# Kernel tuning notes

Measured on AMD Instinct MI355X. Metric: run time of the kernel, lower is better.

## Reference

```python
import jax, jax.numpy as jnp
import numpy as np

N, B, D, K, H = 30000, 16, 32, 8, 8
DIST = 5.0
EPS = 1e-6


def setup_inputs() -> dict:
    key = jax.random.key(0)
    ks = jax.random.split(key, 16)
    sc = 1.0 / np.sqrt(D)
    inp = {
        'pos': jax.random.uniform(ks[0], (N, 3), jnp.float32) * 20.0,
        'node_features': jax.random.normal(ks[1], (N, D), jnp.float32),
        'batch': jnp.sort(jax.random.randint(ks[2], (N,), 0, B, dtype=jnp.int32)),
        'bessel_weights': jnp.linspace(jnp.pi, K * jnp.pi, K).astype(jnp.float32),
        'init_dummy': jax.random.normal(ks[3], (D,), jnp.float32),
        'Wq_dummy': jax.random.normal(ks[4], (D, D), jnp.float32) * sc,
        'Wq_graph': jax.random.normal(ks[5], (D, D), jnp.float32) * sc,
        'Wdot': jax.random.normal(ks[6], (D, D), jnp.float32) * sc,
        'W1_kd': jax.random.normal(ks[7], (K, H), jnp.float32) / np.sqrt(K),
        'W2_kd': jax.random.normal(ks[8], (H, D * D), jnp.float32) / np.sqrt(H),
        'W1_vd': jax.random.normal(ks[9], (K, H), jnp.float32) / np.sqrt(K),
        'W2_vd': jax.random.normal(ks[10], (H, D * D), jnp.float32) / np.sqrt(H),
        'W1_kg': jax.random.normal(ks[11], (K, H), jnp.float32) / np.sqrt(K),
        'W2_kg': jax.random.normal(ks[12], (H, D * D), jnp.float32) / np.sqrt(H),
        'W1_vg': jax.random.normal(ks[13], (K, H), jnp.float32) / np.sqrt(K),
        'W2_vg': jax.random.normal(ks[14], (H, D * D), jnp.float32) / np.sqrt(H),
    }
    return inp


def reference(pos, node_features, batch, bessel_weights, init_dummy,
              Wq_dummy, Wq_graph, Wdot,
              W1_kd, W2_kd, W1_vd, W2_vd, W1_kg, W2_kg, W1_vg, W2_vg):
    scale = 1.0 / np.sqrt(D)

    # --- dummy edge features: per-batch z extents + bessel basis ---
    z = pos[:, 2]                                            # [N]
    z_min = jax.ops.segment_min(z, batch, num_segments=B)    # [B]
    z_max = jax.ops.segment_max(z, batch, num_segments=B)    # [B]
    bot_len = z - z_min[batch] + DIST                        # [N]
    top_len = z_max[batch] + DIST - z                        # [N]

    def bessel(x):  # [N] -> [N,K]
        return jnp.sin(bessel_weights * x[:, None]) / (x[:, None] + EPS)

    edge = jnp.stack([bessel(bot_len), bessel(top_len)], axis=1)  # [N,2,K]

    # --- init dummy node features [B, 2, D] ---
    dummy = jnp.broadcast_to(init_dummy, (B, 2, D))

    def gen_w(W1, W2):  # conditional weight generator (silu MLP)
        return (jax.nn.silu(edge @ W1) @ W2).reshape(N, 2, D, D)

    # --- dummy nodes attend over graph nodes (segment softmax) ---
    wk = gen_w(W1_kd, W2_kd)                                 # [N,2,D,D]
    wv = gen_w(W1_vd, W2_vd)
    q = (dummy @ Wq_dummy)[batch]                            # [N,2,D]
    k = jnp.einsum('nd,nsde->nse', node_features, wk)        # [N,2,D]
    v = jnp.einsum('nd,nsde->nse', node_features, wv)
    s = jnp.einsum('nsq,qk,nsk->ns', q, Wdot, k) * scale     # [N,2]
    m = jax.ops.segment_max(s, batch, num_segments=B)
    e = jnp.exp(s - m[batch])
    zsum = jax.ops.segment_sum(e, batch, num_segments=B)
    attn = e / zsum[batch]                                   # [N,2]
    dummy_new = dummy + jax.ops.segment_sum(attn[..., None] * v, batch, num_segments=B)

    # --- graph nodes attend over (2) dummy nodes ---
    wkg = gen_w(W1_kg, W2_kg)
    wvg = gen_w(W1_vg, W2_vg)
    d_per = dummy_new[batch]                                 # [N,2,D]
    kg = jnp.einsum('nsd,nsde->nse', d_per, wkg)
    vg = jnp.einsum('nsd,nsde->nse', d_per, wvg)
    qg = node_features @ Wq_graph                            # [N,D]
    sg = jnp.einsum('nq,qk,nsk->ns', qg, Wdot, kg) * scale   # [N,2]
    ag = jax.nn.softmax(sg, axis=1)
    x_new = node_features + jnp.einsum('ns,nsd->nd', ag, vg)  # [N,D]
    return x_new
```

## Files before the change

kernel.cpp:

```cpp
#include <hip/hip_runtime.h>
#include <math.h>

#define NN 30000
#define DIST_C 5.0f
#define EPS_C 1e-6f
#define SCALE_C 0.17677669529663687f

#define WS_ZMIN 0
#define WS_ZMAX 16
#define WS_ZSUM 32
#define WS_T    64
#define WS_PK   8256
#define WS_WC   8512

__device__ __forceinline__ float silu(float x) { return x / (1.0f + expf(-x)); }

__device__ __forceinline__ void bessel_edges(float bw0, float x0, float x1, float edge[2][8]) {
    float xs[2]; xs[0] = x0; xs[1] = x1;
#pragma unroll
    for (int s = 0; s < 2; ++s) {
        float x = xs[s];
        float inv = 1.0f / (x + EPS_C);
        float th = bw0 * x;
        float c2 = 2.0f * cosf(th);
        float skm1 = 0.0f;
        float sk = sinf(th);
#pragma unroll
        for (int k = 0; k < 8; ++k) {
            edge[s][k] = sk * inv;
            float nx = c2 * sk - skm1;
            skm1 = sk; sk = nx;
        }
    }
}

__global__ __launch_bounds__(256) void k_pre(const float* __restrict__ pos,
                                             const int* __restrict__ batch,
                                             const float* __restrict__ init_dummy,
                                             const float* __restrict__ Wq_dummy,
                                             const float* __restrict__ Wdot,
                                             const float* __restrict__ W2_kd,
                                             const float* __restrict__ Wq_graph,
                                             float* __restrict__ ws) {
    int t = threadIdx.x, blk = blockIdx.x;
    if (blk < 16) {
        __shared__ int bnd2[2];
        __shared__ float r[8];
        if (t < 2) {
            int target = blk + t;
            int lo = 0, hi = NN;
            while (lo < hi) { int mid = (lo + hi) >> 1; if (batch[mid] < target) lo = mid + 1; else hi = mid; }
            bnd2[t] = lo;
        }
        __syncthreads();
        int s0 = bnd2[0], s1 = bnd2[1];
        float zmn = 3.4e38f, zmx = -3.4e38f;
        for (int i = s0 + t; i < s1; i += 256) {
            float v = pos[3 * i + 2];
            zmn = fminf(zmn, v); zmx = fmaxf(zmx, v);
        }
#pragma unroll
        for (int off = 1; off < 64; off <<= 1) {
            zmn = fminf(zmn, __shfl_xor(zmn, off, 64));
            zmx = fmaxf(zmx, __shfl_xor(zmx, off, 64));
        }
        if ((t & 63) == 0) { r[(t >> 6) * 2] = zmn; r[(t >> 6) * 2 + 1] = zmx; }
        __syncthreads();
        if (t == 0) {
            ws[WS_ZMIN + blk] = fminf(fminf(r[0], r[2]), fminf(r[4], r[6]));
            ws[WS_ZMAX + blk] = fmaxf(fmaxf(r[1], r[3]), fmaxf(r[5], r[7]));
        }
    } else if (blk == 16) {
        __shared__ float qv[32], qW[32];
        if (t < 32) {
            float acc = 0.f;
            for (int d = 0; d < 32; ++d) acc += init_dummy[d] * Wq_dummy[d * 32 + t];
            qv[t] = acc;
        }
        __syncthreads();
        if (t < 32) {
            float acc = 0.f;
            for (int e = 0; e < 32; ++e) acc += qv[e] * Wdot[e * 32 + t];
            qW[t] = acc;
        }
        __syncthreads();
        int h = t >> 5, d = t & 31;
        float acc = 0.f;
        for (int e = 0; e < 32; ++e) acc += W2_kd[h * 1024 + d * 32 + e] * qW[e];
        ws[WS_PK + t] = acc;
    } else if (blk == 17) {
        for (int i = t; i < 1024; i += 256) {
            int d = i >> 5, e = i & 31;
            float acc = 0.f;
            for (int m = 0; m < 32; ++m) acc += Wq_graph[d * 32 + m] * Wdot[m * 32 + e];
            ws[WS_WC + i] = acc;
        }
    } else {
        int idx = blk - 18;
        ws[WS_T + idx * 512 + t] = 0.f;
        ws[WS_T + idx * 512 + 256 + t] = 0.f;
        if (idx == 0 && t < 32) ws[WS_ZSUM + t] = 0.f;
    }
}

__global__ __launch_bounds__(256) void k_phase1(const float* __restrict__ pos,
                                                const int* __restrict__ batch,
                                                const float* __restrict__ nf,
                                                const float* __restrict__ bw,
                                                const float* __restrict__ W1_kd,
                                                const float* __restrict__ W1_vd,
                                                float* __restrict__ ws) {
    __shared__ __align__(16) float Fl[32 * 36];
    __shared__ float Lw[32 * 17];
    __shared__ int   Lb[32];
    __shared__ __align__(16) float Pk[256];
    __shared__ float W1kd[64], W1vd[64], zsl[32];
    int t = threadIdx.x;
    if (t < 64) { W1kd[t] = W1_kd[t]; W1vd[t] = W1_vd[t]; }
    Pk[t] = ws[WS_PK + t];
    if (t < 32) zsl[t] = 0.f;

    int li = t >> 3, g = t & 7;
    int n0 = blockIdx.x * 32;
    int n = n0 + li;
    bool valid = n < NN;
    float4 fv4 = make_float4(0.f, 0.f, 0.f, 0.f);
    int b = 0;
    if (valid) {
        b = batch[n];
        fv4 = ((const float4*)nf)[n * 8 + g];
        ((float4*)(Fl + li * 36))[g] = fv4;
        if (g == 0) Lb[li] = b;
    } else {
        if (g == 0) Lb[li] = -1;
    }
    __syncthreads();

    if (valid) {
        float z = pos[3 * n + 2];
        float zminb = ws[WS_ZMIN + b];
        float zmaxb = ws[WS_ZMAX + b];
        float edge[2][8];
        bessel_edges(bw[0], z - zminb + DIST_C, zmaxb + DIST_C - z, edge);

        float up[8];
        const float4* Pk4 = (const float4*)Pk;
#pragma unroll
        for (int h = 0; h < 8; ++h) {
            float4 p = Pk4[h * 8 + g];
            up[h] = fv4.x * p.x + fv4.y * p.y + fv4.z * p.z + fv4.w * p.w;
        }
        float kd0, kd1;
        {
            float p0 = 0.f, p1 = 0.f;
#pragma unroll
            for (int k = 0; k < 8; ++k) {
                float w = W1kd[k * 8 + g];
                p0 += edge[0][k] * w;
                p1 += edge[1][k] * w;
            }
            kd0 = silu(p0); kd1 = silu(p1);
        }
        int lanebase = (t & 63) & 56;
        float sp0 = 0.f, sp1 = 0.f;
#pragma unroll
        for (int h = 0; h < 8; ++h) {
            sp0 += __shfl(kd0, lanebase + h, 64) * up[h];
            sp1 += __shfl(kd1, lanebase + h, 64) * up[h];
        }
#pragma unroll
        for (int m = 1; m < 8; m <<= 1) {
            sp0 += __shfl_xor(sp0, m, 64);
            sp1 += __shfl_xor(sp1, m, 64);
        }
        float ev0 = expf(sp0 * SCALE_C);
        float ev1 = expf(sp1 * SCALE_C);
        if (g == 0) {
            atomicAdd(&zsl[b * 2 + 0], ev0);
            atomicAdd(&zsl[b * 2 + 1], ev1);
        }
        float q0 = 0.f, q1 = 0.f;
#pragma unroll
        for (int k = 0; k < 8; ++k) {
            float w = W1vd[k * 8 + g];
            q0 += edge[0][k] * w;
            q1 += edge[1][k] * w;
        }
        Lw[li * 17 + g]     = ev0 * silu(q0);
        Lw[li * 17 + 8 + g] = ev1 * silu(q1);
    }
    __syncthreads();
    if (t < 32 && zsl[t] != 0.f) atomicAdd(&ws[WS_ZSUM + t], zsl[t]);

    int count = NN - n0; if (count > 32) count = 32;
    int bf = Lb[0], bl = Lb[count - 1];
    int sh = t & 15, dp = t >> 4;
    for (int b2 = bf; b2 <= bl; ++b2) {
        float a0 = 0.f, a1 = 0.f;
        for (int i = 0; i < count; ++i) {
            if (Lb[i] != b2) continue;
            float w = Lw[i * 17 + sh];
            float2 x = *(const float2*)(Fl + i * 36 + 2 * dp);
            a0 += w * x.x;
            a1 += w * x.y;
        }
        float* Tb = ws + WS_T + b2 * 512 + sh * 32 + 2 * dp;
        atomicAdd(&Tb[0], a0);
        atomicAdd(&Tb[1], a1);
    }
}

__global__ __launch_bounds__(256) void k_fin(const float* __restrict__ pos,
                                             const int* __restrict__ batch,
                                             const float* __restrict__ nf,
                                             const float* __restrict__ bw,
                                             const float* __restrict__ W1_kg,
                                             const float* __restrict__ W1_vg,
                                             const float* __restrict__ init_dummy,
                                             const float* __restrict__ W2_vd,
                                             const float* __restrict__ W2_kg,
                                             const float* __restrict__ W2_vg,
                                             const float* __restrict__ ws,
                                             float* __restrict__ out) {
    __shared__ __align__(16) float Wc[1024];
    __shared__ __align__(16) float Fl[32 * 36];
    __shared__ int   Lb[32];
    __shared__ float W1kg[64], W1vg[64];
    __shared__ float Tl[2][512];
    __shared__ float part[2][512];
    __shared__ float dn[2][64];
    __shared__ __align__(16) float AK[2][512], AV[2][512];

    int t = threadIdx.x;
    int li = t >> 3, g = t & 7;
    int lanebase = (t & 63) & 56;
    for (int i = t; i < 1024; i += 256) Wc[i] = ws[WS_WC + i];
    if (t < 64) { W1kg[t] = W1_kg[t]; W1vg[t] = W1_vg[t]; }

    int n0 = blockIdx.x * 32;
    int n = n0 + li;
    int count = NN - n0; if (count > 32) count = 32;
    bool valid = li < count;
    float4 fv4 = make_float4(0.f, 0.f, 0.f, 0.f);
    float z = 0.f;
    int b = 0;
    if (valid) {
        b = batch[n];
        fv4 = ((const float4*)nf)[n * 8 + g];
        ((float4*)(Fl + li * 36))[g] = fv4;
        z = pos[3 * n + 2];
        if (g == 0) Lb[li] = b;
    }
    __syncthreads();
    int bf = Lb[0], bl = Lb[count - 1];

    Tl[0][t]       = ws[WS_T + bf * 512 + t];
    Tl[0][256 + t] = ws[WS_T + bf * 512 + 256 + t];
    Tl[1][t]       = ws[WS_T + bl * 512 + t];
    Tl[1][256 + t] = ws[WS_T + bl * 512 + 256 + t];
    __syncthreads();
    {
        int h = t >> 5, e = t & 31;
        float a00 = 0.f, a01 = 0.f, a10 = 0.f, a11 = 0.f;
        for (int d = 0; d < 32; ++d) {
            float w2 = W2_vd[h * 1024 + d * 32 + e];
            a00 += Tl[0][h * 32 + d] * w2;
            a01 += Tl[0][256 + h * 32 + d] * w2;
            a10 += Tl[1][h * 32 + d] * w2;
            a11 += Tl[1][256 + h * 32 + d] * w2;
        }
        part[0][t] = a00; part[0][256 + t] = a01;
        part[1][t] = a10; part[1][256 + t] = a11;
    }
    __syncthreads();
    if (t < 64) {
        int s = t >> 5, dd = t & 31;
        float acc0 = 0.f, acc1 = 0.f;
        for (int h = 0; h < 8; ++h) {
            acc0 += part[0][s * 256 + h * 32 + dd];
            acc1 += part[1][s * 256 + h * 32 + dd];
        }
        float id = init_dummy[dd];
        dn[0][t] = id + acc0 / ws[WS_ZSUM + bf * 2 + s];
        dn[1][t] = id + acc1 / ws[WS_ZSUM + bl * 2 + s];
    }
    __syncthreads();
    {
        int h = t >> 5, e = t & 31;
        float k00 = 0.f, k01 = 0.f, k10 = 0.f, k11 = 0.f;
        float v00 = 0.f, v01 = 0.f, v10 = 0.f, v11 = 0.f;
        for (int d = 0; d < 32; ++d) {
            float w2k = W2_kg[h * 1024 + d * 32 + e];
            float w2v = W2_vg[h * 1024 + d * 32 + e];
            k00 += dn[0][d] * w2k;      v00 += dn[0][d] * w2v;
            k01 += dn[0][32 + d] * w2k; v01 += dn[0][32 + d] * w2v;
            k10 += dn[1][d] * w2k;      v10 += dn[1][d] * w2v;
            k11 += dn[1][32 + d] * w2k; v11 += dn[1][32 + d] * w2v;
        }
        AK[0][t] = k00; AK[0][256 + t] = k01;
        AK[1][t] = k10; AK[1][256 + t] = k11;
        AV[0][t] = v00; AV[0][256 + t] = v01;
        AV[1][t] = v10; AV[1][256 + t] = v11;
    }
    __syncthreads();

    if (!valid) return;
    int slot = (b == bf) ? 0 : 1;
    const float4* Ak4 = (const float4*)AK[slot];
    const float4* Av4 = (const float4*)AV[slot];
    const float4* Wc4 = (const float4*)Wc;

    float zminb = ws[WS_ZMIN + b];
    float zmaxb = ws[WS_ZMAX + b];
    float edge[2][8];
    bessel_edges(bw[0], z - zminb + DIST_C, zmaxb + DIST_C - z, edge);

    float sk0, sk1, sv0, sv1;
    {
        float pk0 = 0.f, pk1 = 0.f, pv0 = 0.f, pv1 = 0.f;
#pragma unroll
        for (int k = 0; k < 8; ++k) {
            float wk = W1kg[k * 8 + g];
            float wv = W1vg[k * 8 + g];
            pk0 += edge[0][k] * wk; pk1 += edge[1][k] * wk;
            pv0 += edge[0][k] * wv; pv1 += edge[1][k] * wv;
        }
        sk0 = silu(pk0); sk1 = silu(pk1);
        sv0 = silu(pv0); sv1 = silu(pv1);
    }
    float4 q4 = make_float4(0.f, 0.f, 0.f, 0.f);
    const float* myF = Fl + li * 36;
#pragma unroll
    for (int d = 0; d < 32; ++d) {
        float fd = myF[d];
        float4 w = Wc4[d * 8 + g];
        q4.x += fd * w.x; q4.y += fd * w.y; q4.z += fd * w.z; q4.w += fd * w.w;
    }
    float p0 = 0.f, p1 = 0.f;
#pragma unroll
    for (int h = 0; h < 8; ++h) {
        float4 a0 = Ak4[h * 8 + g];
        float4 a1 = Ak4[64 + h * 8 + g];
        float d0 = q4.x * a0.x + q4.y * a0.y + q4.z * a0.z + q4.w * a0.w;
        float d1 = q4.x * a1.x + q4.y * a1.y + q4.z * a1.z + q4.w * a1.w;
        p0 += __shfl(sk0, lanebase + h, 64) * d0;
        p1 += __shfl(sk1, lanebase + h, 64) * d1;
    }
#pragma unroll
    for (int m = 1; m < 8; m <<= 1) {
        p0 += __shfl_xor(p0, m, 64);
        p1 += __shfl_xor(p1, m, 64);
    }
    float sg0 = p0 * SCALE_C, sg1 = p1 * SCALE_C;
    float mx = fmaxf(sg0, sg1);
    float e0 = expf(sg0 - mx), e1 = expf(sg1 - mx);
    float inv = 1.0f / (e0 + e1);
    float ag0 = e0 * inv, ag1 = e1 * inv;

    float4 x4 = fv4;
#pragma unroll
    for (int h = 0; h < 8; ++h) {
        float w0 = ag0 * __shfl(sv0, lanebase + h, 64);
        float w1 = ag1 * __shfl(sv1, lanebase + h, 64);
        float4 a0 = Av4[h * 8 + g];
        float4 a1 = Av4[64 + h * 8 + g];
        x4.x += w0 * a0.x + w1 * a1.x;
        x4.y += w0 * a0.y + w1 * a1.y;
        x4.z += w0 * a0.z + w1 * a1.z;
        x4.w += w0 * a0.w + w1 * a1.w;
    }
    ((float4*)out)[n * 8 + g] = x4;
}

extern "C" void kernel_launch(void* const* d_in, const int* in_sizes, int n_in,
                              void* d_out, int out_size, void* d_ws, size_t ws_size,
                              hipStream_t stream) {
    const float* pos        = (const float*)d_in[0];
    const float* nf         = (const float*)d_in[1];
    const int*   batch      = (const int*)d_in[2];
    const float* bw         = (const float*)d_in[3];
    const float* init_dummy = (const float*)d_in[4];
    const float* Wq_dummy   = (const float*)d_in[5];
    const float* Wq_graph   = (const float*)d_in[6];
    const float* Wdot       = (const float*)d_in[7];
    const float* W1_kd      = (const float*)d_in[8];
    const float* W2_kd      = (const float*)d_in[9];
    const float* W1_vd      = (const float*)d_in[10];
    const float* W2_vd      = (const float*)d_in[11];
    const float* W1_kg      = (const float*)d_in[12];
    const float* W2_kg      = (const float*)d_in[13];
    const float* W1_vg      = (const float*)d_in[14];
    const float* W2_vg      = (const float*)d_in[15];
    float* ws  = (float*)d_ws;
    float* out = (float*)d_out;

    int nblk = (NN + 31) / 32;
    hipLaunchKernelGGL(k_pre, dim3(34), dim3(256), 0, stream,
                       pos, batch, init_dummy, Wq_dummy, Wdot, W2_kd, Wq_graph, ws);
    hipLaunchKernelGGL(k_phase1, dim3(nblk), dim3(256), 0, stream,
                       pos, batch, nf, bw, W1_kd, W1_vd, ws);
    hipLaunchKernelGGL(k_fin, dim3(nblk), dim3(256), 0, stream,
                       pos, batch, nf, bw, W1_kg, W1_vg, init_dummy,
                       W2_vd, W2_kg, W2_vg, ws, out);
}
```

Baseline: 124.0 us.

## Halve node tile per block and skip duplicate dummy-segment recompute

Both the phase1 and final kernels now handle 16 nodes per block with 128 threads instead of 32 nodes with 256 threads. This doubles the grid size, and bounds checks are dropped because N divides evenly by 16. The final kernel computes the per-block dummy-node chain (T·W2_vd, then dn, then K/V through W2_kg/W2_vg) only for the segments actually present, usually one instead of always two. It reuses two scratch buffers in place of four shared arrays, which cuts shared memory. The phase1 scatter now uses float4 loads and four atomics per thread. The trade-off is that more blocks each redo the per-segment matvec work, so total redundant weight reads may rise even though each block does less.

```diff
diff --git a/kernel.cpp b/kernel.cpp
--- a/kernel.cpp
+++ b/kernel.cpp
@@ -12,6 +12,8 @@
 #define WS_T    64
 #define WS_PK   8256
 #define WS_WC   8512
+
+#define NPT 16
 
 __device__ __forceinline__ float silu(float x) { return x / (1.0f + expf(-x)); }
 
@@ -103,40 +105,34 @@
     }
 }
 
-__global__ __launch_bounds__(256) void k_phase1(const float* __restrict__ pos,
+__global__ __launch_bounds__(128) void k_phase1(const float* __restrict__ pos,
                                                 const int* __restrict__ batch,
                                                 const float* __restrict__ nf,
                                                 const float* __restrict__ bw,
                                                 const float* __restrict__ W1_kd,
                                                 const float* __restrict__ W1_vd,
                                                 float* __restrict__ ws) {
-    __shared__ __align__(16) float Fl[32 * 36];
-    __shared__ float Lw[32 * 17];
-    __shared__ int   Lb[32];
+    __shared__ __align__(16) float Fl[NPT * 36];
+    __shared__ float Lw[NPT * 17];
+    __shared__ int   Lb[NPT];
     __shared__ __align__(16) float Pk[256];
     __shared__ float W1kd[64], W1vd[64], zsl[32];
     int t = threadIdx.x;
     if (t < 64) { W1kd[t] = W1_kd[t]; W1vd[t] = W1_vd[t]; }
     Pk[t] = ws[WS_PK + t];
+    Pk[t + 128] = ws[WS_PK + t + 128];
     if (t < 32) zsl[t] = 0.f;
 
     int li = t >> 3, g = t & 7;
-    int n0 = blockIdx.x * 32;
+    int n0 = blockIdx.x * NPT;
     int n = n0 + li;
-    bool valid = n < NN;
-    float4 fv4 = make_float4(0.f, 0.f, 0.f, 0.f);
-    int b = 0;
-    if (valid) {
-        b = batch[n];
-        fv4 = ((const float4*)nf)[n * 8 + g];
-        ((float4*)(Fl + li * 36))[g] = fv4;
-        if (g == 0) Lb[li] = b;
-    } else {
-        if (g == 0) Lb[li] = -1;
-    }
-    __syncthreads();
-
-    if (valid) {
+    int b = batch[n];
+    float4 fv4 = ((const float4*)nf)[n * 8 + g];
+    ((float4*)(Fl + li * 36))[g] = fv4;
+    if (g == 0) Lb[li] = b;
+    __syncthreads();
+
+    {
         float z = pos[3 * n + 2];
         float zminb = ws[WS_ZMIN + b];
         float zmaxb = ws[WS_ZMAX + b];
@@ -192,25 +188,24 @@
     __syncthreads();
     if (t < 32 && zsl[t] != 0.f) atomicAdd(&ws[WS_ZSUM + t], zsl[t]);
 
-    int count = NN - n0; if (count > 32) count = 32;
-    int bf = Lb[0], bl = Lb[count - 1];
-    int sh = t & 15, dp = t >> 4;
+    int bf = Lb[0], bl = Lb[NPT - 1];
+    int sh = t & 15, dq = t >> 4;
+    const float4* Fl4 = (const float4*)Fl;
     for (int b2 = bf; b2 <= bl; ++b2) {
-        float a0 = 0.f, a1 = 0.f;
-        for (int i = 0; i < count; ++i) {
+        float4 a = make_float4(0.f, 0.f, 0.f, 0.f);
+        for (int i = 0; i < NPT; ++i) {
             if (Lb[i] != b2) continue;
             float w = Lw[i * 17 + sh];
-            float2 x = *(const float2*)(Fl + i * 36 + 2 * dp);
-            a0 += w * x.x;
-            a1 += w * x.y;
-        }
-        float* Tb = ws + WS_T + b2 * 512 + sh * 32 + 2 * dp;
-        atomicAdd(&Tb[0], a0);
-        atomicAdd(&Tb[1], a1);
-    }
-}
-
-__global__ __launch_bounds__(256) void k_fin(const float* __restrict__ pos,
+            float4 x = Fl4[i * 9 + dq];
+            a.x += w * x.x; a.y += w * x.y; a.z += w * x.z; a.w += w * x.w;
+        }
+        float* Tb = ws + WS_T + b2 * 512 + sh * 32 + dq * 4;
+        atomicAdd(&Tb[0], a.x); atomicAdd(&Tb[1], a.y);
+        atomicAdd(&Tb[2], a.z); atomicAdd(&Tb[3], a.w);
+    }
+}
+
+__global__ __launch_bounds__(128) void k_fin(const float* __restrict__ pos,
                                              const int* __restrict__ batch,
                                              const float* __restrict__ nf,
                                              const float* __restrict__ bw,
@@ -223,91 +218,87 @@
                                              const float* __restrict__ ws,
                                              float* __restrict__ out) {
     __shared__ __align__(16) float Wc[1024];
-    __shared__ __align__(16) float Fl[32 * 36];
-    __shared__ int   Lb[32];
+    __shared__ __align__(16) float Fl[NPT * 36];
+    __shared__ int   Lb[NPT];
     __shared__ float W1kg[64], W1vg[64];
-    __shared__ float Tl[2][512];
-    __shared__ float part[2][512];
+    __shared__ __align__(16) float scr0[2][512];
+    __shared__ __align__(16) float scr1[2][512];
     __shared__ float dn[2][64];
-    __shared__ __align__(16) float AK[2][512], AV[2][512];
 
     int t = threadIdx.x;
     int li = t >> 3, g = t & 7;
     int lanebase = (t & 63) & 56;
-    for (int i = t; i < 1024; i += 256) Wc[i] = ws[WS_WC + i];
+    {
+        const float4* Wg4 = (const float4*)(ws + WS_WC);
+        float4* Wc4w = (float4*)Wc;
+        Wc4w[t] = Wg4[t];
+        Wc4w[t + 128] = Wg4[t + 128];
+    }
     if (t < 64) { W1kg[t] = W1_kg[t]; W1vg[t] = W1_vg[t]; }
 
-    int n0 = blockIdx.x * 32;
+    int n0 = blockIdx.x * NPT;
     int n = n0 + li;
-    int count = NN - n0; if (count > 32) count = 32;
-    bool valid = li < count;
-    float4 fv4 = make_float4(0.f, 0.f, 0.f, 0.f);
-    float z = 0.f;
-    int b = 0;
-    if (valid) {
-        b = batch[n];
-        fv4 = ((const float4*)nf)[n * 8 + g];
-        ((float4*)(Fl + li * 36))[g] = fv4;
-        z = pos[3 * n + 2];
-        if (g == 0) Lb[li] = b;
-    }
-    __syncthreads();
-    int bf = Lb[0], bl = Lb[count - 1];
-
-    Tl[0][t]       = ws[WS_T + bf * 512 + t];
-    Tl[0][256 + t] = ws[WS_T + bf * 512 + 256 + t];
-    Tl[1][t]       = ws[WS_T + bl * 512 + t];
-    Tl[1][256 + t] = ws[WS_T + bl * 512 + 256 + t];
-    __syncthreads();
-    {
-        int h = t >> 5, e = t & 31;
-        float a00 = 0.f, a01 = 0.f, a10 = 0.f, a11 = 0.f;
-        for (int d = 0; d < 32; ++d) {
-            float w2 = W2_vd[h * 1024 + d * 32 + e];
-            a00 += Tl[0][h * 32 + d] * w2;
-            a01 += Tl[0][256 + h * 32 + d] * w2;
-            a10 += Tl[1][h * 32 + d] * w2;
-            a11 += Tl[1][256 + h * 32 + d] * w2;
-        }
-        part[0][t] = a00; part[0][256 + t] = a01;
-        part[1][t] = a10; part[1][256 + t] = a11;
+    int b = batch[n];
+    float4 fv4 = ((const float4*)nf)[n * 8 + g];
+    ((float4*)(Fl + li * 36))[g] = fv4;
+    float z = pos[3 * n + 2];
+    if (g == 0) Lb[li] = b;
+    __syncthreads();
+    int bf = Lb[0], bl = Lb[NPT - 1];
+    int nseg = (bl != bf) ? 2 : 1;
+
+    for (int sl = 0; sl < nseg; ++sl) {
+        const float* Tg = ws + WS_T + (sl ? bl : bf) * 512;
+        scr0[sl][t]       = Tg[t];
+        scr0[sl][t + 128] = Tg[t + 128];
+        scr0[sl][t + 256] = Tg[t + 256];
+        scr0[sl][t + 384] = Tg[t + 384];
+    }
+    __syncthreads();
+    for (int sl = 0; sl < nseg; ++sl) {
+        for (int o = t; o < 256; o += 128) {
+            int h = o >> 5, e = o & 31;
+            float a0 = 0.f, a1 = 0.f;
+            for (int d = 0; d < 32; ++d) {
+                float w2 = W2_vd[h * 1024 + d * 32 + e];
+                a0 += scr0[sl][h * 32 + d] * w2;
+                a1 += scr0[sl][256 + h * 32 + d] * w2;
+            }
+            scr1[sl][o] = a0; scr1[sl][256 + o] = a1;
+        }
     }
     __syncthreads();
     if (t < 64) {
         int s = t >> 5, dd = t & 31;
-        float acc0 = 0.f, acc1 = 0.f;
-        for (int h = 0; h < 8; ++h) {
-            acc0 += part[0][s * 256 + h * 32 + dd];
-            acc1 += part[1][s * 256 + h * 32 + dd];
-        }
         float id = init_dummy[dd];
-        dn[0][t] = id + acc0 / ws[WS_ZSUM + bf * 2 + s];
-        dn[1][t] = id + acc1 / ws[WS_ZSUM + bl * 2 + s];
-    }
-    __syncthreads();
-    {
-        int h = t >> 5, e = t & 31;
-        float k00 = 0.f, k01 = 0.f, k10 = 0.f, k11 = 0.f;
-        float v00 = 0.f, v01 = 0.f, v10 = 0.f, v11 = 0.f;
-        for (int d = 0; d < 32; ++d) {
-            float w2k = W2_kg[h * 1024 + d * 32 + e];
-            float w2v = W2_vg[h * 1024 + d * 32 + e];
-            k00 += dn[0][d] * w2k;      v00 += dn[0][d] * w2v;
-            k01 += dn[0][32 + d] * w2k; v01 += dn[0][32 + d] * w2v;
-            k10 += dn[1][d] * w2k;      v10 += dn[1][d] * w2v;
-            k11 += dn[1][32 + d] * w2k; v11 += dn[1][32 + d] * w2v;
-        }
-        AK[0][t] = k00; AK[0][256 + t] = k01;
-        AK[1][t] = k10; AK[1][256 + t] = k11;
-        AV[0][t] = v00; AV[0][256 + t] = v01;
-        AV[1][t] = v10; AV[1][256 + t] = v11;
-    }
-    __syncthreads();
-
-    if (!valid) return;
+        for (int sl = 0; sl < nseg; ++sl) {
+            int bb = sl ? bl : bf;
+            float acc = 0.f;
+            for (int h = 0; h < 8; ++h) acc += scr1[sl][s * 256 + h * 32 + dd];
+            dn[sl][t] = id + acc / ws[WS_ZSUM + bb * 2 + s];
+        }
+    }
+    __syncthreads();
+    for (int sl = 0; sl < nseg; ++sl) {
+        for (int o = t; o < 256; o += 128) {
+            int h = o >> 5, e = o & 31;
+            float k0 = 0.f, k1 = 0.f, v0 = 0.f, v1 = 0.f;
+            for (int d = 0; d < 32; ++d) {
+                float w2k = W2_kg[h * 1024 + d * 32 + e];
+                float w2v = W2_vg[h * 1024 + d * 32 + e];
+                float d0 = dn[sl][d], d1 = dn[sl][32 + d];
+                k0 += d0 * w2k; k1 += d1 * w2k;
+                v0 += d0 * w2v; v1 += d1 * w2v;
+            }
+            scr0[sl][o] = k0; scr0[sl][256 + o] = k1;
+            scr1[sl][o] = v0; scr1[sl][256 + o] = v1;
+        }
+    }
+    __syncthreads();
+
     int slot = (b == bf) ? 0 : 1;
-    const float4* Ak4 = (const float4*)AK[slot];
-    const float4* Av4 = (const float4*)AV[slot];
+    const float4* Ak4 = (const float4*)scr0[slot];
+    const float4* Av4 = (const float4*)scr1[slot];
     const float4* Wc4 = (const float4*)Wc;
 
     float zminb = ws[WS_ZMIN + b];
@@ -394,12 +385,12 @@
     float* ws  = (float*)d_ws;
     float* out = (float*)d_out;
 
-    int nblk = (NN + 31) / 32;
+    int nblk = NN / NPT;
     hipLaunchKernelGGL(k_pre, dim3(34), dim3(256), 0, stream,
                        pos, batch, init_dummy, Wq_dummy, Wdot, W2_kd, Wq_graph, ws);
-    hipLaunchKernelGGL(k_phase1, dim3(nblk), dim3(256), 0, stream,
+    hipLaunchKernelGGL(k_phase1, dim3(nblk), dim3(128), 0, stream,
                        pos, batch, nf, bw, W1_kd, W1_vd, ws);
-    hipLaunchKernelGGL(k_fin, dim3(nblk), dim3(256), 0, stream,
+    hipLaunchKernelGGL(k_fin, dim3(nblk), dim3(128), 0, stream,
                        pos, batch, nf, bw, W1_kg, W1_vg, init_dummy,
                        W2_vd, W2_kg, W2_vg, ws, out);
 }
```

Result: slower. 154.6 us (+24.7%).

## Hoist per-batch dummy-node K/V computation into a separate small kernel

Applied to the files above, without the earlier changes.

The per-batch dummy update and the graph-side K/V projections were recomputed redundantly in every k_fin block (about 938 blocks, each doing matvecs against W2_vd, W2_kg and W2_vg). They are now computed once per (batch, side) pair by a new 32-block k_batch kernel, which stores them in the workspace. k_fin only loads the one or two precomputed 512-float slices it needs, and the Wc load becomes a float4 copy. This adds one extra kernel launch and a global round trip in exchange for removing the redundant weight reads and FLOPs.

```diff
diff --git a/kernel.cpp b/kernel.cpp
--- a/kernel.cpp
+++ b/kernel.cpp
@@ -12,6 +12,10 @@
 #define WS_T    64
 #define WS_PK   8256
 #define WS_WC   8512
+#define WS_AKG  9536
+#define WS_AVG  17728
+
+#define NPT 32
 
 __device__ __forceinline__ float silu(float x) { return x / (1.0f + expf(-x)); }
 
@@ -110,9 +114,9 @@
                                                 const float* __restrict__ W1_kd,
                                                 const float* __restrict__ W1_vd,
                                                 float* __restrict__ ws) {
-    __shared__ __align__(16) float Fl[32 * 36];
-    __shared__ float Lw[32 * 17];
-    __shared__ int   Lb[32];
+    __shared__ __align__(16) float Fl[NPT * 36];
+    __shared__ float Lw[NPT * 17];
+    __shared__ int   Lb[NPT];
     __shared__ __align__(16) float Pk[256];
     __shared__ float W1kd[64], W1vd[64], zsl[32];
     int t = threadIdx.x;
@@ -121,7 +125,7 @@
     if (t < 32) zsl[t] = 0.f;
 
     int li = t >> 3, g = t & 7;
-    int n0 = blockIdx.x * 32;
+    int n0 = blockIdx.x * NPT;
     int n = n0 + li;
     bool valid = n < NN;
     float4 fv4 = make_float4(0.f, 0.f, 0.f, 0.f);
@@ -192,7 +196,7 @@
     __syncthreads();
     if (t < 32 && zsl[t] != 0.f) atomicAdd(&ws[WS_ZSUM + t], zsl[t]);
 
-    int count = NN - n0; if (count > 32) count = 32;
+    int count = NN - n0; if (count > NPT) count = NPT;
     int bf = Lb[0], bl = Lb[count - 1];
     int sh = t & 15, dp = t >> 4;
     for (int b2 = bf; b2 <= bl; ++b2) {
@@ -210,36 +214,75 @@
     }
 }
 
+__global__ __launch_bounds__(256) void k_batch(const float* __restrict__ init_dummy,
+                                               const float* __restrict__ W2_vd,
+                                               const float* __restrict__ W2_kg,
+                                               const float* __restrict__ W2_vg,
+                                               float* __restrict__ ws) {
+    int bs = blockIdx.x;
+    int b = bs >> 1, s = bs & 1;
+    int t = threadIdx.x;
+    __shared__ float Tl[256];
+    __shared__ float part[256];
+    __shared__ float dn[32];
+    Tl[t] = ws[WS_T + b * 512 + s * 256 + t];
+    __syncthreads();
+    {
+        int h = t >> 5, e = t & 31;
+        float acc = 0.f;
+#pragma unroll
+        for (int d = 0; d < 32; ++d) acc += Tl[h * 32 + d] * W2_vd[h * 1024 + d * 32 + e];
+        part[t] = acc;
+    }
+    __syncthreads();
+    if (t < 32) {
+        float acc = 0.f;
+#pragma unroll
+        for (int h = 0; h < 8; ++h) acc += part[h * 32 + t];
+        float zs = ws[WS_ZSUM + b * 2 + s];
+        dn[t] = init_dummy[t] + acc / zs;
+    }
+    __syncthreads();
+    {
+        int h = t >> 5, e = t & 31;
+        float ak = 0.f, av = 0.f;
+#pragma unroll
+        for (int d = 0; d < 32; ++d) {
+            float dv = dn[d];
+            ak += dv * W2_kg[h * 1024 + d * 32 + e];
+            av += dv * W2_vg[h * 1024 + d * 32 + e];
+        }
+        ws[WS_AKG + b * 512 + s * 256 + t] = ak;
+        ws[WS_AVG + b * 512 + s * 256 + t] = av;
+    }
+}
+
 __global__ __launch_bounds__(256) void k_fin(const float* __restrict__ pos,
                                              const int* __restrict__ batch,
                                              const float* __restrict__ nf,
                                              const float* __restrict__ bw,
                                              const float* __restrict__ W1_kg,
                                              const float* __restrict__ W1_vg,
-                                             const float* __restrict__ init_dummy,
-                                             const float* __restrict__ W2_vd,
-                                             const float* __restrict__ W2_kg,
-                                             const float* __restrict__ W2_vg,
                                              const float* __restrict__ ws,
                                              float* __restrict__ out) {
     __shared__ __align__(16) float Wc[1024];
-    __shared__ __align__(16) float Fl[32 * 36];
-    __shared__ int   Lb[32];
+    __shared__ __align__(16) float Fl[NPT * 36];
+    __shared__ int   Lb[NPT];
     __shared__ float W1kg[64], W1vg[64];
-    __shared__ float Tl[2][512];
-    __shared__ float part[2][512];
-    __shared__ float dn[2][64];
     __shared__ __align__(16) float AK[2][512], AV[2][512];
 
     int t = threadIdx.x;
     int li = t >> 3, g = t & 7;
     int lanebase = (t & 63) & 56;
-    for (int i = t; i < 1024; i += 256) Wc[i] = ws[WS_WC + i];
+    {
+        const float4* Wg4 = (const float4*)(ws + WS_WC);
+        ((float4*)Wc)[t] = Wg4[t];
+    }
     if (t < 64) { W1kg[t] = W1_kg[t]; W1vg[t] = W1_vg[t]; }
 
-    int n0 = blockIdx.x * 32;
+    int n0 = blockIdx.x * NPT;
     int n = n0 + li;
-    int count = NN - n0; if (count > 32) count = 32;
+    int count = NN - n0; if (count > NPT) count = NPT;
     bool valid = li < count;
     float4 fv4 = make_float4(0.f, 0.f, 0.f, 0.f);
     float z = 0.f;
@@ -253,54 +296,14 @@
     }
     __syncthreads();
     int bf = Lb[0], bl = Lb[count - 1];
-
-    Tl[0][t]       = ws[WS_T + bf * 512 + t];
-    Tl[0][256 + t] = ws[WS_T + bf * 512 + 256 + t];
-    Tl[1][t]       = ws[WS_T + bl * 512 + t];
-    Tl[1][256 + t] = ws[WS_T + bl * 512 + 256 + t];
-    __syncthreads();
-    {
-        int h = t >> 5, e = t & 31;
-        float a00 = 0.f, a01 = 0.f, a10 = 0.f, a11 = 0.f;
-        for (int d = 0; d < 32; ++d) {
-            float w2 = W2_vd[h * 1024 + d * 32 + e];
-            a00 += Tl[0][h * 32 + d] * w2;
-            a01 += Tl[0][256 + h * 32 + d] * w2;
-            a10 += Tl[1][h * 32 + d] * w2;
-            a11 += Tl[1][256 + h * 32 + d] * w2;
-        }
-        part[0][t] = a00; part[0][256 + t] = a01;
-        part[1][t] = a10; part[1][256 + t] = a11;
-    }
-    __syncthreads();
-    if (t < 64) {
-        int s = t >> 5, dd = t & 31;
-        float acc0 = 0.f, acc1 = 0.f;
-        for (int h = 0; h < 8; ++h) {
-            acc0 += part[0][s * 256 + h * 32 + dd];
-            acc1 += part[1][s * 256 + h * 32 + dd];
-        }
-        float id = init_dummy[dd];
-        dn[0][t] = id + acc0 / ws[WS_ZSUM + bf * 2 + s];
-        dn[1][t] = id + acc1 / ws[WS_ZSUM + bl * 2 + s];
-    }
-    __syncthreads();
-    {
-        int h = t >> 5, e = t & 31;
-        float k00 = 0.f, k01 = 0.f, k10 = 0.f, k11 = 0.f;
-        float v00 = 0.f, v01 = 0.f, v10 = 0.f, v11 = 0.f;
-        for (int d = 0; d < 32; ++d) {
-            float w2k = W2_kg[h * 1024 + d * 32 + e];
-            float w2v = W2_vg[h * 1024 + d * 32 + e];
-            k00 += dn[0][d] * w2k;      v00 += dn[0][d] * w2v;
-            k01 += dn[0][32 + d] * w2k; v01 += dn[0][32 + d] * w2v;
-            k10 += dn[1][d] * w2k;      v10 += dn[1][d] * w2v;
-            k11 += dn[1][32 + d] * w2k; v11 += dn[1][32 + d] * w2v;
-        }
-        AK[0][t] = k00; AK[0][256 + t] = k01;
-        AK[1][t] = k10; AK[1][256 + t] = k11;
-        AV[0][t] = v00; AV[0][256 + t] = v01;
-        AV[1][t] = v10; AV[1][256 + t] = v11;
+    int nseg = (bl != bf) ? 2 : 1;
+
+    for (int sl = 0; sl < nseg; ++sl) {
+        int bb = sl ? bl : bf;
+        const float4* Ag = (const float4*)(ws + WS_AKG + bb * 512);
+        const float4* Vg = (const float4*)(ws + WS_AVG + bb * 512);
+        if (t < 128) ((float4*)AK[sl])[t] = Ag[t];
+        else         ((float4*)AV[sl])[t - 128] = Vg[t - 128];
     }
     __syncthreads();
 
@@ -394,12 +397,13 @@
     float* ws  = (float*)d_ws;
     float* out = (float*)d_out;
 
-    int nblk = (NN + 31) / 32;
+    int nblk = (NN + NPT - 1) / NPT;
     hipLaunchKernelGGL(k_pre, dim3(34), dim3(256), 0, stream,
                        pos, batch, init_dummy, Wq_dummy, Wdot, W2_kd, Wq_graph, ws);
     hipLaunchKernelGGL(k_phase1, dim3(nblk), dim3(256), 0, stream,
                        pos, batch, nf, bw, W1_kd, W1_vd, ws);
+    hipLaunchKernelGGL(k_batch, dim3(32), dim3(256), 0, stream,
+                       init_dummy, W2_vd, W2_kg, W2_vg, ws);
     hipLaunchKernelGGL(k_fin, dim3(nblk), dim3(256), 0, stream,
-                       pos, batch, nf, bw, W1_kg, W1_vg, init_dummy,
-                       W2_vd, W2_kg, W2_vg, ws, out);
-}
+                       pos, batch, nf, bw, W1_kg, W1_vg, ws, out);
+}
```

Measured after the change: 122.9 us. About the same (-0.8%).
